# Kernel optimization log

Hardware: AMD Instinct MI355X
Metric: run time of the kernel (lower is better)

The kernel has to match this reference:

```python
import jax, jax.numpy as jnp
import numpy as np

B, S, D = 1, 2048, 2048
H = 16
HD = D // H           # 128
FFN_H = 5632          # int(2*4*D/3) rounded up to multiple of 256
EPS = 1e-5
ROPE_THETA = 10000.0


def rms_norm(x, w, eps=EPS):
    # x * rsqrt(mean(x^2, -1) + eps) * w
    return x * jax.lax.rsqrt(jnp.mean(x * x, axis=-1, keepdims=True) + eps) * w


def apply_rope(x, cos, sin):
    # x: [B, S, H, HD]; cos/sin: [S, HD//2]
    b, s, h, hd = x.shape
    xr = x.reshape(b, s, h, hd // 2, 2)
    x_re, x_im = xr[..., 0], xr[..., 1]
    c = cos[None, :, None, :]
    sn = sin[None, :, None, :]
    o_re = x_re * c - x_im * sn
    o_im = x_re * sn + x_im * c
    return jnp.stack([o_re, o_im], axis=-1).reshape(b, s, h, hd)


def setup_inputs() -> dict:
    key = jax.random.key(0)
    ks = jax.random.split(key, 10)
    x = jax.random.normal(ks[0], (B, S, D), dtype=jnp.float32)
    # RoPE frequencies (Llama-style)
    inv_freq = 1.0 / (ROPE_THETA ** (np.arange(0, HD, 2, dtype=np.float32) / HD))
    angles = np.outer(np.arange(S, dtype=np.float32), inv_freq)  # [S, HD//2]
    freqs_cos = jnp.asarray(np.cos(angles), dtype=jnp.float32)
    freqs_sin = jnp.asarray(np.sin(angles), dtype=jnp.float32)
    # causal mask: 1 = keep, 0 = masked
    mask = jnp.tril(jnp.ones((S, S), dtype=jnp.int32))[None, None]
    sc = 0.02
    return {
        "x": x,
        "freqs_cos": freqs_cos,
        "freqs_sin": freqs_sin,
        "mask": mask,
        "wq": jax.random.normal(ks[1], (D, D), jnp.float32) * sc,
        "wk": jax.random.normal(ks[2], (D, D), jnp.float32) * sc,
        "wv": jax.random.normal(ks[3], (D, D), jnp.float32) * sc,
        "wo": jax.random.normal(ks[4], (D, D), jnp.float32) * sc,
        "w1": jax.random.normal(ks[5], (D, FFN_H), jnp.float32) * sc,
        "w2": jax.random.normal(ks[6], (FFN_H, D), jnp.float32) * sc,
        "w3": jax.random.normal(ks[7], (D, FFN_H), jnp.float32) * sc,
        "attn_norm_w": jnp.ones((D,), jnp.float32),
        "ffn_norm_w": jnp.ones((D,), jnp.float32),
    }


def reference(x, freqs_cos, freqs_sin, mask, wq, wk, wv, wo, w1, w2, w3,
              attn_norm_w, ffn_norm_w):
    b, s, d = x.shape
    # --- attention block ---
    xn = rms_norm(x, attn_norm_w)
    q = (xn @ wq).reshape(b, s, H, HD)
    k = (xn @ wk).reshape(b, s, H, HD)
    v = (xn @ wv).reshape(b, s, H, HD)
    q = apply_rope(q, freqs_cos, freqs_sin)
    k = apply_rope(k, freqs_cos, freqs_sin)
    scores = jnp.einsum('bqhd,bkhd->bhqk', q, k) / jnp.sqrt(jnp.float32(HD))
    scores = jnp.where(mask == 0, -jnp.inf, scores)
    probs = jax.nn.softmax(scores, axis=-1)
    attn = jnp.einsum('bhqk,bkhd->bqhd', probs, v).reshape(b, s, d)
    h = x + attn @ wo
    # --- SwiGLU FFN block ---
    hn = rms_norm(h, ffn_norm_w)
    ff = (jax.nn.silu(hn @ w1) * (hn @ w3)) @ w2
    return h + ff
```

## Files before the change

kernel.cpp:

```cpp
#include <hip/hip_runtime.h>
#include <hip/hip_bf16.h>

typedef __bf16 bf16x8 __attribute__((ext_vector_type(8)));
typedef float f32x4 __attribute__((ext_vector_type(4)));
typedef unsigned short u16x8 __attribute__((ext_vector_type(8)));
typedef unsigned short u16x4 __attribute__((ext_vector_type(4)));

#define DEV static __device__ __forceinline__

DEV unsigned short f2bf(float f) {
    unsigned u = __builtin_bit_cast(unsigned, f);
    u += 0x7fffu + ((u >> 16) & 1u);
    return (unsigned short)(u >> 16);
}
DEV float bf2f(unsigned short h) {
    unsigned u = ((unsigned)h) << 16;
    return __builtin_bit_cast(float, u);
}

DEV void gl2lds16(const void* g, void* l) {
    __builtin_amdgcn_global_load_lds(
        (const __attribute__((address_space(1))) void*)g,
        (__attribute__((address_space(3))) void*)l, 16, 0, 0);
}

#define WAITV(N) asm volatile("s_waitcnt vmcnt(" #N ")" ::: "memory")
#define SBAR()   asm volatile("s_barrier" ::: "memory")

#define STAGE128D(KT, BUF)                                                    \
    _Pragma("unroll")                                                         \
    for (int sl = 0; sl < 3; ++sl) {                                          \
        const unsigned short* sbase = (sl == 0)                               \
            ? A  + (size_t)bm * K                                             \
            : BT + (size_t)(bn + (sl - 1) * 128) * K;                         \
        _Pragma("unroll")                                                     \
        for (int j = 0; j < 2; ++j) {                                         \
            const unsigned short* g = sbase + (size_t)(srow + j * 64) * K     \
                                      + koff + (KT) * 64 + lc;                \
            gl2lds16(g, &lds[BUF][sl][wave * 512 + j * 4096]);                \
        }                                                                     \
    }

#define DSREAD128(BUF)                                                        \
    {                                                                         \
        const char* Ab = (const char*)&lds[BUF][0][0];                        \
        const char* Bb = (const char*)&lds[BUF][1 + (wn >> 1)][0];            \
        _Pragma("unroll")                                                     \
        for (int m4 = 0; m4 < 4; ++m4)                                        \
            _Pragma("unroll")                                                 \
            for (int kk = 0; kk < 2; ++kk)                                    \
                a_[m4][kk] = *(const bf16x8*)(Ab +                            \
                    (wm * 64 + m4 * 16 + lr) * 128 +                          \
                    ((kk * 64 + lg * 16) ^ xsw));                             \
        _Pragma("unroll")                                                     \
        for (int n2 = 0; n2 < 4; ++n2)                                        \
            _Pragma("unroll")                                                 \
            for (int kk = 0; kk < 2; ++kk)                                    \
                b_[n2][kk] = *(const bf16x8*)(Bb +                            \
                    ((wn & 1) * 64 + n2 * 16 + lr) * 128 +                    \
                    ((kk * 64 + lg * 16) ^ xsw));                             \
    }

#define MFMA128                                                               \
    __builtin_amdgcn_s_setprio(1);                                            \
    _Pragma("unroll")                                                         \
    for (int m4 = 0; m4 < 4; ++m4)                                            \
        _Pragma("unroll")                                                     \
        for (int n2 = 0; n2 < 4; ++n2)                                        \
            _Pragma("unroll")                                                 \
            for (int kk = 0; kk < 2; ++kk)                                    \
                acc[m4][n2] = __builtin_amdgcn_mfma_f32_16x16x32_bf16(        \
                    a_[m4][kk], b_[n2][kk], acc[m4][n2], 0, 0, 0);            \
    __builtin_amdgcn_s_setprio(0);

template <int EPI>
__global__ __launch_bounds__(512, 2)
void gemm128d(const unsigned short* __restrict__ A,
              const unsigned short* __restrict__ BT,
              unsigned short* __restrict__ outB,
              float* __restrict__ outP,
              int M, int N, int K,
              const float* __restrict__ cs, const float* __restrict__ sn,
              unsigned short* __restrict__ vT)
{
    __shared__ alignas(16) unsigned short lds[3][3][8192];
    const int tid  = threadIdx.x;
    const int lane = tid & 63;
    const int wave = tid >> 6;
    const int wm = wave >> 2;
    const int wn = wave & 3;
    const int lr = lane & 15;
    const int lg = lane >> 4;
    const int gy  = gridDim.y;
    const int lin = blockIdx.y * gridDim.x + blockIdx.x;
    const int cpx = (gridDim.x * gy) >> 3;
    const int swz = (lin & 7) * cpx + (lin >> 3);
    const int bm = (swz % gy) * 128;
    const int bn = (swz / gy) * 256;
    const int xsw  = (lr & 7) << 4;
    const int srow = tid >> 3;
    const int lc   = ((tid & 7) ^ (srow & 7)) * 8;
    int koff, NT;
    if constexpr (EPI == 1 || EPI == 3) {
        const int Kh = K >> 1; koff = blockIdx.z * Kh; NT = Kh >> 6;
    } else {
        koff = 0; NT = K >> 6;
    }

    f32x4 acc[4][4] = {};
    bf16x8 a_[4][2], b_[4][2];

    STAGE128D(0, 0);
    STAGE128D(1, 1);
    WAITV(6); SBAR();
    DSREAD128(0);

    int bc = 0;
    for (int kt = 0; kt < NT - 2; ++kt) {
        const int nb = (bc == 0) ? 2 : bc - 1;
        STAGE128D(kt + 2, nb);
        MFMA128;
        WAITV(6); SBAR();
        const int rb = (bc == 2) ? 0 : bc + 1;
        DSREAD128(rb);
        bc = rb;
    }
    MFMA128;
    WAITV(0); SBAR();
    {
        const int rb = (bc == 2) ? 0 : bc + 1;
        DSREAD128(rb);
    }
    MFMA128;

#pragma unroll
    for (int m4 = 0; m4 < 4; ++m4) {
        const int row = bm + wm * 64 + m4 * 16 + lg * 4;
#pragma unroll
        for (int n2 = 0; n2 < 4; ++n2) {
            const int col = bn + wn * 64 + n2 * 16 + lr;
            if constexpr (EPI == 4) {
                if (bn >= 4096) {
                    u16x4 o;
#pragma unroll
                    for (int r = 0; r < 4; ++r) o[r] = f2bf(acc[m4][n2][r]);
                    *(u16x4*)(vT + (size_t)(col - 4096) * 2048 + row) = o;
                } else {
#pragma unroll
                    for (int r = 0; r < 4; ++r) {
                        const float v  = acc[m4][n2][r];
                        const float vo = __shfl_xor(v, 1);
                        const int rr = row + r;
                        const int i0 = (col & 127) >> 1;
                        const float c = cs[rr * 64 + i0];
                        const float s = sn[rr * 64 + i0];
                        const float o = (lr & 1) ? (vo * s + v * c)
                                                 : (v * c - vo * s);
                        outB[(size_t)rr * N + col] = f2bf(o);
                    }
                }
            } else {
#pragma unroll
                for (int r = 0; r < 4; ++r) {
                    if constexpr (EPI == 1) {
                        outP[(size_t)blockIdx.z * M * N + (size_t)(row + r) * N + col] = acc[m4][n2][r];
                    } else if constexpr (EPI == 3) {
                        unsafeAtomicAdd(&outP[(size_t)(row + r) * N + col], acc[m4][n2][r]);
                    } else {
                        const float v  = acc[m4][n2][r];
                        const float vo = __shfl_xor(v, 1);
                        const float x1 = (lr & 1) ? vo : v;
                        const float x3 = (lr & 1) ? v : vo;
                        const float g  = x1 / (1.0f + __expf(-x1)) * x3;
                        if (!(lr & 1))
                            outB[(size_t)(row + r) * (N >> 1) + (col >> 1)] = f2bf(g);
                    }
                }
            }
        }
    }
}

__global__ __launch_bounds__(256)
void reduce2_norm(const float* __restrict__ res, const float* __restrict__ p,
                  const float* __restrict__ w, float* __restrict__ hout,
                  unsigned short* __restrict__ nout)
{
    const int row = blockIdx.x, tid = threadIdx.x;
    const float4* r4 = (const float4*)(res + (size_t)row * 2048);
    const float4* a4 = (const float4*)(p   + (size_t)row * 2048);
    const float4* b4 = (const float4*)(p + (size_t)2048 * 2048 + (size_t)row * 2048);
    float4* h4 = (float4*)(hout + (size_t)row * 2048);
    float4 h[2];
    float ss = 0.f;
#pragma unroll
    for (int i = 0; i < 2; ++i) {
        const int idx = i * 256 + tid;
        const float4 r = r4[idx], a = a4[idx], b = b4[idx];
        float4 v = make_float4(r.x + a.x + b.x, r.y + a.y + b.y,
                               r.z + a.z + b.z, r.w + a.w + b.w);
        h[i] = v; h4[idx] = v;
        ss += v.x * v.x + v.y * v.y + v.z * v.z + v.w * v.w;
    }
#pragma unroll
    for (int off = 32; off; off >>= 1) ss += __shfl_xor(ss, off);
    __shared__ float red[4];
    if ((tid & 63) == 0) red[tid >> 6] = ss;
    __syncthreads();
    const float tot = red[0] + red[1] + red[2] + red[3];
    const float sc = rsqrtf(tot * (1.0f / 2048.0f) + 1e-5f);
#pragma unroll
    for (int i = 0; i < 2; ++i) {
        const int idx = i * 256 + tid;
        const float4 wv = ((const float4*)w)[idx];
        u16x4 o;
        o[0] = f2bf(h[i].x * sc * wv.x); o[1] = f2bf(h[i].y * sc * wv.y);
        o[2] = f2bf(h[i].z * sc * wv.z); o[3] = f2bf(h[i].w * sc * wv.w);
        *(u16x4*)(nout + (size_t)row * 2048 + idx * 4) = o;
    }
}

__global__ __launch_bounds__(256)
void rmsnorm_kernel(const float* __restrict__ x, const float* __restrict__ w,
                    unsigned short* __restrict__ out)
{
    const int row = blockIdx.x;
    const int tid = threadIdx.x;
    const float* xr = x + (size_t)row * 2048;
    const float4 a = *reinterpret_cast<const float4*>(xr + tid * 8);
    const float4 b = *reinterpret_cast<const float4*>(xr + tid * 8 + 4);
    float ss = a.x * a.x + a.y * a.y + a.z * a.z + a.w * a.w
             + b.x * b.x + b.y * b.y + b.z * b.z + b.w * b.w;
#pragma unroll
    for (int off = 32; off; off >>= 1) ss += __shfl_xor(ss, off);
    __shared__ float red[4];
    if ((tid & 63) == 0) red[tid >> 6] = ss;
    __syncthreads();
    const float tot = red[0] + red[1] + red[2] + red[3];
    const float sc = rsqrtf(tot * (1.0f / 2048.0f) + 1e-5f);
    const float4 wa = *reinterpret_cast<const float4*>(w + tid * 8);
    const float4 wb = *reinterpret_cast<const float4*>(w + tid * 8 + 4);
    u16x8 o;
    o[0] = f2bf(a.x * sc * wa.x); o[1] = f2bf(a.y * sc * wa.y);
    o[2] = f2bf(a.z * sc * wa.z); o[3] = f2bf(a.w * sc * wa.w);
    o[4] = f2bf(b.x * sc * wb.x); o[5] = f2bf(b.y * sc * wb.y);
    o[6] = f2bf(b.z * sc * wb.z); o[7] = f2bf(b.w * sc * wb.w);
    *reinterpret_cast<u16x8*>(out + (size_t)row * 2048 + tid * 8) = o;
}

DEV void convT_half(const float* __restrict__ w, unsigned short* __restrict__ wT,
                    int K, int N, int rmul, int radd, int bk, int bn,
                    int tid, unsigned short (*t)[66])
{
    const int r = tid >> 4, c4 = (tid & 15) * 4;
#pragma unroll
    for (int i = 0; i < 4; ++i) {
        const int row = r + i * 16;
        const float4 v = *reinterpret_cast<const float4*>(w + (size_t)(bk + row) * N + bn + c4);
        t[row][c4 + 0] = f2bf(v.x); t[row][c4 + 1] = f2bf(v.y);
        t[row][c4 + 2] = f2bf(v.z); t[row][c4 + 3] = f2bf(v.w);
    }
    __syncthreads();
#pragma unroll
    for (int i = 0; i < 4; ++i) {
        const int n = r + i * 16;
        u16x4 o;
#pragma unroll
        for (int e = 0; e < 4; ++e) o[e] = t[c4 + e][n];
        *reinterpret_cast<u16x4*>(wT + (size_t)(rmul * (bn + n) + radd) * K + bk + c4) = o;
    }
}

__global__ __launch_bounds__(256)
void convT3_kernel(const float* __restrict__ w0, const float* __restrict__ w1,
                   const float* __restrict__ w2v, unsigned short* __restrict__ wT)
{
    __shared__ unsigned short t[64][66];
    const int z = blockIdx.z;
    const float* w = (z == 0) ? w0 : (z == 1) ? w1 : w2v;
    convT_half(w, wT + (size_t)z * 2048 * 2048, 2048, 2048, 1, 0,
               blockIdx.y * 64, blockIdx.x * 64, threadIdx.x, t);
}

__global__ __launch_bounds__(512)
void flash_mega(const unsigned short* __restrict__ q,
                const unsigned short* __restrict__ k,
                const unsigned short* __restrict__ vT,
                unsigned short* __restrict__ attn,
                const float* __restrict__ wo, const float* __restrict__ w1,
                const float* __restrict__ w3, const float* __restrict__ w2,
                unsigned short* __restrict__ woT,
                unsigned short* __restrict__ w13T,
                unsigned short* __restrict__ w2T)
{
    __shared__ alignas(16) unsigned short Ks[2][64][136];
    __shared__ alignas(16) unsigned short Vs[2][128][72];
    __shared__ alignas(16) unsigned short Ps[8][16][72];
    __shared__ unsigned short tbuf[2][64][66];

    const int bid = blockIdx.x;
    const int tid = threadIdx.x;

    if (bid >= 256) {
        const int half = tid >> 8;
        const int t256 = tid & 255;
        if (bid < 768) {
            const int t2 = (bid - 256) * 2 + half;
            convT_half(wo, woT, 2048, 2048, 1, 0,
                       (t2 >> 5) * 64, (t2 & 31) * 64, t256, tbuf[half]);
        } else if (bid < 3584) {
            const int t2 = (bid - 768) * 2 + half;
            const int z  = t2 / 2816;
            const int rm = t2 % 2816;
            convT_half(z ? w3 : w1, w13T, 2048, 5632, 2, z,
                       (rm / 88) * 64, (rm % 88) * 64, t256, tbuf[half]);
        } else {
            const int t2 = (bid - 3584) * 2 + half;
            convT_half(w2, w2T, 5632, 2048, 1, 0,
                       (t2 / 32) * 64, (t2 % 32) * 64, t256, tbuf[half]);
        }
        return;
    }

    const int hh = bid >> 4;
    const int pi = bid & 15;
    const int lane = tid & 63, wave = tid >> 6;
    const int qt = (wave >> 2) ? (31 - pi) : pi;
    const int lr = lane & 15, lg = lane >> 4;
    const int q0 = qt * 64 + (wave & 3) * 16;
    const int myNT = qt + 1;
    const int NT   = 32 - pi;

    const int kr0 = tid >> 4, kc0 = (tid & 15) * 8;
    const int vr0 = tid >> 3, vc0 = (tid & 7) * 8;

    bf16x8 qf[4];
#pragma unroll
    for (int c = 0; c < 4; ++c)
        qf[c] = *reinterpret_cast<const bf16x8*>(
            q + (size_t)(q0 + lr) * 6144 + hh * 128 + c * 32 + lg * 8);

    f32x4 oacc[8] = {};
    float m_r[4], l_r[4];
#pragma unroll
    for (int r = 0; r < 4; ++r) { m_r[r] = -INFINITY; l_r[r] = 0.0f; }
    const float scale = 0.08838834764831845f;

    u16x8 kreg0, kreg1, vreg0, vreg1;
    auto gload = [&](int kt) {
        const int kv0 = kt * 64;
        kreg0 = *reinterpret_cast<const u16x8*>(k + (size_t)(kv0 + kr0) * 6144 + hh * 128 + kc0);
        kreg1 = *reinterpret_cast<const u16x8*>(k + (size_t)(kv0 + kr0 + 32) * 6144 + hh * 128 + kc0);
        vreg0 = *reinterpret_cast<const u16x8*>(vT + (size_t)(hh * 128 + vr0) * 2048 + kv0 + vc0);
        vreg1 = *reinterpret_cast<const u16x8*>(vT + (size_t)(hh * 128 + vr0 + 64) * 2048 + kv0 + vc0);
    };
    auto lwrite = [&](int buf) {
        *reinterpret_cast<u16x8*>(&Ks[buf][kr0][kc0])      = kreg0;
        *reinterpret_cast<u16x8*>(&Ks[buf][kr0 + 32][kc0]) = kreg1;
        *reinterpret_cast<u16x8*>(&Vs[buf][vr0][vc0])      = vreg0;
        *reinterpret_cast<u16x8*>(&Vs[buf][vr0 + 64][vc0]) = vreg1;
    };

    gload(0); lwrite(0);
    __syncthreads();

    for (int kt = 0; kt < NT; ++kt) {
        const int buf = kt & 1;
        if (kt + 1 < NT) gload(kt + 1);

        if (kt < myNT) {
            const int kv0 = kt * 64;
            const bool masked = (kt == myNT - 1);
            f32x4 s[4] = {};
            __builtin_amdgcn_s_setprio(1);
#pragma unroll
            for (int ct = 0; ct < 4; ++ct)
#pragma unroll
                for (int c = 0; c < 4; ++c) {
                    const bf16x8 kf = *reinterpret_cast<const bf16x8*>(
                        &Ks[buf][ct * 16 + lr][c * 32 + lg * 8]);
                    s[ct] = __builtin_amdgcn_mfma_f32_16x16x32_bf16(qf[c], kf, s[ct], 0, 0, 0);
                }
            __builtin_amdgcn_s_setprio(0);
#pragma unroll
            for (int ct = 0; ct < 4; ++ct)
#pragma unroll
                for (int r = 0; r < 4; ++r) {
                    float v = s[ct][r] * scale;
                    if (masked) {
                        const int kvg = kv0 + ct * 16 + lr;
                        const int qg  = q0 + lg * 4 + r;
                        if (kvg > qg) v = -INFINITY;
                    }
                    s[ct][r] = v;
                }
            float mn[4], alpha[4], rs[4];
#pragma unroll
            for (int r = 0; r < 4; ++r) {
                float v = fmaxf(fmaxf(s[0][r], s[1][r]), fmaxf(s[2][r], s[3][r]));
                v = fmaxf(v, __shfl_xor(v, 1));
                v = fmaxf(v, __shfl_xor(v, 2));
                v = fmaxf(v, __shfl_xor(v, 4));
                v = fmaxf(v, __shfl_xor(v, 8));
                mn[r] = fmaxf(m_r[r], v);
                alpha[r] = __expf(m_r[r] - mn[r]);
                m_r[r] = mn[r];
                rs[r] = 0.0f;
            }
#pragma unroll
            for (int ct = 0; ct < 4; ++ct)
#pragma unroll
                for (int r = 0; r < 4; ++r) {
                    const float p = __expf(s[ct][r] - mn[r]);
                    s[ct][r] = p;
                    rs[r] += p;
                }
#pragma unroll
            for (int r = 0; r < 4; ++r) {
                float t2 = rs[r];
                t2 += __shfl_xor(t2, 1);
                t2 += __shfl_xor(t2, 2);
                t2 += __shfl_xor(t2, 4);
                t2 += __shfl_xor(t2, 8);
                l_r[r] = l_r[r] * alpha[r] + t2;
            }
#pragma unroll
            for (int ot = 0; ot < 8; ++ot)
#pragma unroll
                for (int r = 0; r < 4; ++r) oacc[ot][r] *= alpha[r];

#pragma unroll
            for (int ct = 0; ct < 4; ++ct)
#pragma unroll
                for (int r = 0; r < 4; ++r)
                    Ps[wave][lg * 4 + r][ct * 16 + lr] = f2bf(s[ct][r]);

            __builtin_amdgcn_s_setprio(1);
#pragma unroll
            for (int c2 = 0; c2 < 2; ++c2) {
                const bf16x8 pf = *reinterpret_cast<const bf16x8*>(
                    &Ps[wave][lr][c2 * 32 + lg * 8]);
#pragma unroll
                for (int ot = 0; ot < 8; ++ot) {
                    const bf16x8 vf = *reinterpret_cast<const bf16x8*>(
                        &Vs[buf][ot * 16 + lr][c2 * 32 + lg * 8]);
                    oacc[ot] = __builtin_amdgcn_mfma_f32_16x16x32_bf16(pf, vf, oacc[ot], 0, 0, 0);
                }
            }
            __builtin_amdgcn_s_setprio(0);
        }

        if (kt + 1 < NT) lwrite(buf ^ 1);
        __syncthreads();
    }

#pragma unroll
    for (int ot = 0; ot < 8; ++ot)
#pragma unroll
        for (int r = 0; r < 4; ++r) {
            const float v = oacc[ot][r] / l_r[r];
            attn[(size_t)(q0 + lg * 4 + r) * 2048 + hh * 128 + ot * 16 + lr] = f2bf(v);
        }
}

extern "C" void kernel_launch(void* const* d_in, const int* in_sizes, int n_in,
                              void* d_out, int out_size, void* d_ws, size_t ws_size,
                              hipStream_t stream)
{
    const float* x    = (const float*)d_in[0];
    const float* fcos = (const float*)d_in[1];
    const float* fsin = (const float*)d_in[2];
    const float* wq  = (const float*)d_in[4];
    const float* wk  = (const float*)d_in[5];
    const float* wv  = (const float*)d_in[6];
    const float* wo  = (const float*)d_in[7];
    const float* w1  = (const float*)d_in[8];
    const float* w2  = (const float*)d_in[9];
    const float* w3  = (const float*)d_in[10];
    const float* anw = (const float*)d_in[11];
    const float* fnw = (const float*)d_in[12];
    float* out = (float*)d_out;

    char* ws = (char*)d_ws;
    size_t off = 0;
    auto alloc = [&](size_t bytes) { void* p = ws + off; off += bytes; return p; };
    const size_t SZ_DD = (size_t)2048 * 2048 * 2;
    const size_t SZ_DF = (size_t)2048 * 5632 * 2;

    unsigned short* qkvoT = (unsigned short*)alloc(4 * SZ_DD);
    unsigned short* w13T  = (unsigned short*)alloc(2 * SZ_DF);
    unsigned short* w2T   = (unsigned short*)alloc(SZ_DF);

    char* reg1 = (char*)alloc((size_t)48 * 1024 * 1024);
    unsigned short* xn   = (unsigned short*)reg1;
    unsigned short* qkv  = (unsigned short*)(reg1 + SZ_DD);
    unsigned short* vTb  = (unsigned short*)(reg1 + SZ_DD + 3 * SZ_DD);
    unsigned short* ab   = (unsigned short*)(reg1 + SZ_DD + 4 * SZ_DD);
    float*          pk   = (float*)reg1;
    unsigned short* hn   = (unsigned short*)(reg1 + 4 * SZ_DD);

    char* reg2 = (char*)alloc(SZ_DF);
    unsigned short* t1 = (unsigned short*)reg2;

    convT3_kernel<<<dim3(32, 32, 3), 256, 0, stream>>>(wq, wk, wv, qkvoT);

    rmsnorm_kernel<<<2048, 256, 0, stream>>>(x, anw, xn);
    gemm128d<4><<<dim3(24, 16), 512, 0, stream>>>(xn, qkvoT, qkv, nullptr,
                                                  2048, 6144, 2048, fcos, fsin, vTb);
    flash_mega<<<4992, 512, 0, stream>>>(qkv, qkv + 2048, vTb, ab,
                                         wo, w1, w3, w2,
                                         qkvoT + 3 * (size_t)2048 * 2048, w13T, w2T);
    gemm128d<1><<<dim3(8, 16, 2), 512, 0, stream>>>(ab, qkvoT + 3 * (size_t)2048 * 2048,
                                                    nullptr, pk, 2048, 2048, 2048,
                                                    nullptr, nullptr, nullptr);
    reduce2_norm<<<2048, 256, 0, stream>>>(x, pk, fnw, out, hn);

    gemm128d<2><<<dim3(44, 16), 512, 0, stream>>>(hn, w13T, t1, nullptr,
                                                  2048, 11264, 2048,
                                                  nullptr, nullptr, nullptr);
    gemm128d<3><<<dim3(8, 16, 2), 512, 0, stream>>>(t1, w2T, nullptr, out,
                                                    2048, 2048, 5632,
                                                    nullptr, nullptr, nullptr);
}
```

Baseline: 423.9 us.

## Use persistent grid-stride loop with prefetch for weight transposes in flash kernel

```diff
diff --git a/kernel.cpp b/kernel.cpp
--- a/kernel.cpp
+++ b/kernel.cpp
@@ -282,6 +282,28 @@
                blockIdx.y * 64, blockIdx.x * 64, threadIdx.x, t);
 }
 
+DEV void ct_decode(int t2,
+                   const float* wo, const float* w1, const float* w3,
+                   const float* w2,
+                   unsigned short* woT, unsigned short* w13T, unsigned short* w2T,
+                   const float*& w, unsigned short*& wT,
+                   int& K, int& N, int& rmul, int& radd, int& bk, int& bn)
+{
+    if (t2 < 1024) {
+        w = wo; wT = woT; K = 2048; N = 2048; rmul = 1; radd = 0;
+        bk = (t2 >> 5) * 64; bn = (t2 & 31) * 64;
+    } else if (t2 < 6656) {
+        const int u = t2 - 1024;
+        const int z = u / 2816, rm = u % 2816;
+        w = z ? w3 : w1; wT = w13T; K = 2048; N = 5632; rmul = 2; radd = z;
+        bk = (rm / 88) * 64; bn = (rm % 88) * 64;
+    } else {
+        const int u = t2 - 6656;
+        w = w2; wT = w2T; K = 5632; N = 2048; rmul = 1; radd = 0;
+        bk = (u / 32) * 64; bn = (u % 32) * 64;
+    }
+}
+
 __global__ __launch_bounds__(512)
 void flash_mega(const unsigned short* __restrict__ q,
                 const unsigned short* __restrict__ k,
@@ -296,7 +318,6 @@
     __shared__ alignas(16) unsigned short Ks[2][64][136];
     __shared__ alignas(16) unsigned short Vs[2][128][72];
     __shared__ alignas(16) unsigned short Ps[8][16][72];
-    __shared__ unsigned short tbuf[2][64][66];
 
     const int bid = blockIdx.x;
     const int tid = threadIdx.x;
@@ -304,20 +325,67 @@
     if (bid >= 256) {
         const int half = tid >> 8;
         const int t256 = tid & 255;
-        if (bid < 768) {
-            const int t2 = (bid - 256) * 2 + half;
-            convT_half(wo, woT, 2048, 2048, 1, 0,
-                       (t2 >> 5) * 64, (t2 & 31) * 64, t256, tbuf[half]);
-        } else if (bid < 3584) {
-            const int t2 = (bid - 768) * 2 + half;
-            const int z  = t2 / 2816;
-            const int rm = t2 % 2816;
-            convT_half(z ? w3 : w1, w13T, 2048, 5632, 2, z,
-                       (rm / 88) * 64, (rm % 88) * 64, t256, tbuf[half]);
-        } else {
-            const int t2 = (bid - 3584) * 2 + half;
-            convT_half(w2, w2T, 5632, 2048, 1, 0,
-                       (t2 / 32) * 64, (t2 % 32) * 64, t256, tbuf[half]);
+        const int gid  = (bid - 256) * 2 + half;
+        const int r = t256 >> 4, c4 = (t256 & 15) * 4;
+        unsigned short (*tb)[66] =
+            (unsigned short (*)[66])(&Ks[0][0][0] + half * 64 * 66);
+        const int TOT = 9472;
+
+        float4 cur[4], nxt[4];
+        const float* wC; unsigned short* wTC;
+        int KC, NC, rmC, raC, bkC, bnC;
+        int t2 = gid;
+        bool act = (t2 < TOT);
+        if (act) {
+            ct_decode(t2, wo, w1, w3, w2, woT, w13T, w2T,
+                      wC, wTC, KC, NC, rmC, raC, bkC, bnC);
+#pragma unroll
+            for (int i = 0; i < 4; ++i)
+                cur[i] = *(const float4*)(wC + (size_t)(bkC + r + i * 16) * NC + bnC + c4);
+        }
+#pragma unroll 1
+        for (int it = 0; it < 10; ++it) {
+            const int t2n = t2 + 1024;
+            const bool actn = (t2n < TOT);
+            const float* wN; unsigned short* wTN;
+            int KN, NN, rmN, raN, bkN, bnN;
+            if (actn) {
+                ct_decode(t2n, wo, w1, w3, w2, woT, w13T, w2T,
+                          wN, wTN, KN, NN, rmN, raN, bkN, bnN);
+#pragma unroll
+                for (int i = 0; i < 4; ++i)
+                    nxt[i] = *(const float4*)(wN + (size_t)(bkN + r + i * 16) * NN + bnN + c4);
+            }
+            if (act) {
+#pragma unroll
+                for (int i = 0; i < 4; ++i) {
+                    const int row = r + i * 16;
+                    tb[row][c4 + 0] = f2bf(cur[i].x);
+                    tb[row][c4 + 1] = f2bf(cur[i].y);
+                    tb[row][c4 + 2] = f2bf(cur[i].z);
+                    tb[row][c4 + 3] = f2bf(cur[i].w);
+                }
+            }
+            __syncthreads();
+            if (act) {
+#pragma unroll
+                for (int i = 0; i < 4; ++i) {
+                    const int n = r + i * 16;
+                    u16x4 o;
+#pragma unroll
+                    for (int e = 0; e < 4; ++e) o[e] = tb[c4 + e][n];
+                    *reinterpret_cast<u16x4*>(
+                        wTC + (size_t)(rmC * (bnC + n) + raC) * KC + bkC + c4) = o;
+                }
+            }
+            __syncthreads();
+            t2 = t2n; act = actn;
+            if (actn) {
+                wC = wN; wTC = wTN; KC = KN; NC = NN;
+                rmC = rmN; raC = raN; bkC = bkN; bnC = bnN;
+#pragma unroll
+                for (int i = 0; i < 4; ++i) cur[i] = nxt[i];
+            }
         }
         return;
     }
@@ -507,9 +575,9 @@
     rmsnorm_kernel<<<2048, 256, 0, stream>>>(x, anw, xn);
     gemm128d<4><<<dim3(24, 16), 512, 0, stream>>>(xn, qkvoT, qkv, nullptr,
                                                   2048, 6144, 2048, fcos, fsin, vTb);
-    flash_mega<<<4992, 512, 0, stream>>>(qkv, qkv + 2048, vTb, ab,
-                                         wo, w1, w3, w2,
-                                         qkvoT + 3 * (size_t)2048 * 2048, w13T, w2T);
+    flash_mega<<<768, 512, 0, stream>>>(qkv, qkv + 2048, vTb, ab,
+                                        wo, w1, w3, w2,
+                                        qkvoT + 3 * (size_t)2048 * 2048, w13T, w2T);
     gemm128d<1><<<dim3(8, 16, 2), 512, 0, stream>>>(ab, qkvoT + 3 * (size_t)2048 * 2048,
                                                     nullptr, pk, 2048, 2048, 2048,
                                                     nullptr, nullptr, nullptr);
```

Result: no change. 424.1 us (+0.0%).
